# Kernel optimization log

Hardware: AMD Instinct MI355X
Metric: run time of the kernel (lower is better)

The kernel has to match this reference:

```python
import jax, jax.numpy as jnp
import numpy as np

K = 3  # kernel_size
PAD = K // 2


def setup_inputs() -> dict:
    key = jax.random.key(0)
    k1, k2 = jax.random.split(key)
    B, C, H, W = 8, 64, 128, 128
    x = jax.random.normal(k1, (B, C, H, W), dtype=jnp.float32)
    dynamic_kernel = jax.random.normal(k2, (B, C, K * K, H, W), dtype=jnp.float32)
    return {"x": x, "dynamic_kernel": dynamic_kernel}


def reference(x, dynamic_kernel):
    # x: [B,C,H,W]; dynamic_kernel: [B,C,K^2,H,W]
    B, C, H, W = x.shape
    xp = jnp.pad(x, ((0, 0), (0, 0), (PAD, PAD), (PAD, PAD)))
    # F.unfold patch ordering: (ki, kj) row-major, matching view(B,C,K*K,H,W)
    patches = jnp.stack(
        [xp[:, :, i:i + H, j:j + W] for i in range(K) for j in range(K)],
        axis=2,
    )  # [B,C,K^2,H,W]
    out = (patches * dynamic_kernel).sum(axis=2)  # [B,C,H,W]
    return out
```

## Files before the change

kernel.cpp:

```cpp
#include <hip/hip_runtime.h>


constexpr int Bc = 8, Cc = 64, Hc = 128, Wc = 128;
constexpr int HW = Hc * Wc;

__global__ __launch_bounds__(256) void adaconv2d_kernel(
    const float* __restrict__ x,
    const float* __restrict__ dk,
    float* __restrict__ out)
{
    int tid = blockIdx.x * blockDim.x + threadIdx.x;
    int w0   = (tid & 31) << 2;
    int rest = tid >> 5;
    int h    = rest & (Hc - 1);
    int bc   = rest >> 7;

    const float* xp = x + bc * HW;
    const float* kp = dk + (long long)bc * 9 * HW + h * Wc + w0;

    float xr[3][6];
    #pragma unroll
    for (int r = 0; r < 3; ++r) {
        int hh = h + r - 1;
        if (hh >= 0 && hh < Hc) {
            const float* row = xp + hh * Wc;
            float4 m = *reinterpret_cast<const float4*>(row + w0);
            xr[r][1] = m.x; xr[r][2] = m.y; xr[r][3] = m.z; xr[r][4] = m.w;
            xr[r][0] = (w0 > 0)        ? row[w0 - 1] : 0.f;
            xr[r][5] = (w0 + 4 < Wc)   ? row[w0 + 4] : 0.f;
        } else {
            #pragma unroll
            for (int j = 0; j < 6; ++j) xr[r][j] = 0.f;
        }
    }

    float4 acc = make_float4(0.f, 0.f, 0.f, 0.f);
    #pragma unroll
    for (int r = 0; r < 3; ++r) {
        #pragma unroll
        for (int s = 0; s < 3; ++s) {
            float4 k = *reinterpret_cast<const float4*>(kp + (r * 3 + s) * HW);
            acc.x += xr[r][s + 0] * k.x;
            acc.y += xr[r][s + 1] * k.y;
            acc.z += xr[r][s + 2] * k.z;
            acc.w += xr[r][s + 3] * k.w;
        }
    }

    *reinterpret_cast<float4*>(out + bc * HW + h * Wc + w0) = acc;
}

extern "C" void kernel_launch(void* const* d_in, const int* in_sizes, int n_in,
                              void* d_out, int out_size, void* d_ws, size_t ws_size,
                              hipStream_t stream) {
    const float* x  = (const float*)d_in[0];
    const float* dk = (const float*)d_in[1];
    float* out      = (float*)d_out;

    const int total_quads = Bc * Cc * Hc * (Wc / 4);
    const int block = 256;
    const int grid  = total_quads / block;
    adaconv2d_kernel<<<grid, block, 0, stream>>>(x, dk, out);
}
```

Before: 413.8 us.

## Process 16 outputs per thread with nontemporal kernel loads and output stores

Each thread now computes 8 contiguous columns for two rows 16 apart, and each block covers a 32-row chunk of one channel plane. The dynamic kernel weights are read and the outputs written with nontemporal builtins to avoid polluting cache with streamed data. The aim is more bytes in flight per thread and fewer redundant halo loads. The trade-off is four times fewer threads and higher register use, which may reduce occupancy.

```diff
diff --git a/kernel.cpp b/kernel.cpp
--- a/kernel.cpp
+++ b/kernel.cpp
@@ -3,51 +3,97 @@
 
 constexpr int Bc = 8, Cc = 64, Hc = 128, Wc = 128;
 constexpr int HW = Hc * Wc;
+constexpr int ROWS = 32;
+constexpr int CHUNKS = Hc / ROWS;
+
+typedef float f32x4 __attribute__((ext_vector_type(4)));
+
+__device__ __forceinline__ void load_xrows(const float* __restrict__ xp,
+                                           int R, int w0, float xr[3][10]) {
+    #pragma unroll
+    for (int r = 0; r < 3; ++r) {
+        int hh = R + r - 1;
+        if (hh >= 0 && hh < Hc) {
+            const float* row = xp + hh * Wc;
+            f32x4 m0 = *reinterpret_cast<const f32x4*>(row + w0);
+            f32x4 m1 = *reinterpret_cast<const f32x4*>(row + w0 + 4);
+            xr[r][1] = m0.x; xr[r][2] = m0.y; xr[r][3] = m0.z; xr[r][4] = m0.w;
+            xr[r][5] = m1.x; xr[r][6] = m1.y; xr[r][7] = m1.z; xr[r][8] = m1.w;
+            xr[r][0] = (w0 > 0)      ? row[w0 - 1] : 0.f;
+            xr[r][9] = (w0 + 8 < Wc) ? row[w0 + 8] : 0.f;
+        } else {
+            #pragma unroll
+            for (int q = 0; q < 10; ++q) xr[r][q] = 0.f;
+        }
+    }
+}
 
 __global__ __launch_bounds__(256) void adaconv2d_kernel(
     const float* __restrict__ x,
     const float* __restrict__ dk,
     float* __restrict__ out)
 {
-    int tid = blockIdx.x * blockDim.x + threadIdx.x;
-    int w0   = (tid & 31) << 2;
-    int rest = tid >> 5;
-    int h    = rest & (Hc - 1);
-    int bc   = rest >> 7;
+    int i  = threadIdx.x;
+    int j  = i & 15;
+    int p  = i >> 4;
+    int w0 = j << 3;
+
+    int blk = blockIdx.x;
+    int cb  = blk & (CHUNKS - 1);
+    int bc  = blk >> 2;
+
+    int R0 = cb * ROWS + p;
+    int R1 = R0 + 16;
 
     const float* xp = x + bc * HW;
-    const float* kp = dk + (long long)bc * 9 * HW + h * Wc + w0;
+    const float* kb = dk + (long long)bc * 9 * HW;
 
-    float xr[3][6];
+    float xa[3][10], xb[3][10];
+    load_xrows(xp, R0, w0, xa);
+    load_xrows(xp, R1, w0, xb);
+
+    float a0[8], a1[8];
     #pragma unroll
-    for (int r = 0; r < 3; ++r) {
-        int hh = h + r - 1;
-        if (hh >= 0 && hh < Hc) {
-            const float* row = xp + hh * Wc;
-            float4 m = *reinterpret_cast<const float4*>(row + w0);
-            xr[r][1] = m.x; xr[r][2] = m.y; xr[r][3] = m.z; xr[r][4] = m.w;
-            xr[r][0] = (w0 > 0)        ? row[w0 - 1] : 0.f;
-            xr[r][5] = (w0 + 4 < Wc)   ? row[w0 + 4] : 0.f;
-        } else {
-            #pragma unroll
-            for (int j = 0; j < 6; ++j) xr[r][j] = 0.f;
-        }
+    for (int q = 0; q < 8; ++q) { a0[q] = 0.f; a1[q] = 0.f; }
+
+    #pragma unroll
+    for (int t = 0; t < 9; ++t) {
+        const int r = t / 3, s = t - 3 * r;
+        const float* kt = kb + t * HW;
+        f32x4 k0a = __builtin_nontemporal_load(reinterpret_cast<const f32x4*>(kt + R0 * Wc + w0));
+        f32x4 k0b = __builtin_nontemporal_load(reinterpret_cast<const f32x4*>(kt + R0 * Wc + w0 + 4));
+        f32x4 k1a = __builtin_nontemporal_load(reinterpret_cast<const f32x4*>(kt + R1 * Wc + w0));
+        f32x4 k1b = __builtin_nontemporal_load(reinterpret_cast<const f32x4*>(kt + R1 * Wc + w0 + 4));
+
+        a0[0] += xa[r][s + 0] * k0a.x;
+        a0[1] += xa[r][s + 1] * k0a.y;
+        a0[2] += xa[r][s + 2] * k0a.z;
+        a0[3] += xa[r][s + 3] * k0a.w;
+        a0[4] += xa[r][s + 4] * k0b.x;
+        a0[5] += xa[r][s + 5] * k0b.y;
+        a0[6] += xa[r][s + 6] * k0b.z;
+        a0[7] += xa[r][s + 7] * k0b.w;
+
+        a1[0] += xb[r][s + 0] * k1a.x;
+        a1[1] += xb[r][s + 1] * k1a.y;
+        a1[2] += xb[r][s + 2] * k1a.z;
+        a1[3] += xb[r][s + 3] * k1a.w;
+        a1[4] += xb[r][s + 4] * k1b.x;
+        a1[5] += xb[r][s + 5] * k1b.y;
+        a1[6] += xb[r][s + 6] * k1b.z;
+        a1[7] += xb[r][s + 7] * k1b.w;
     }
 
-    float4 acc = make_float4(0.f, 0.f, 0.f, 0.f);
-    #pragma unroll
-    for (int r = 0; r < 3; ++r) {
-        #pragma unroll
-        for (int s = 0; s < 3; ++s) {
-            float4 k = *reinterpret_cast<const float4*>(kp + (r * 3 + s) * HW);
-            acc.x += xr[r][s + 0] * k.x;
-            acc.y += xr[r][s + 1] * k.y;
-            acc.z += xr[r][s + 2] * k.z;
-            acc.w += xr[r][s + 3] * k.w;
-        }
-    }
-
-    *reinterpret_cast<float4*>(out + bc * HW + h * Wc + w0) = acc;
+    float* o0 = out + bc * HW + R0 * Wc + w0;
+    float* o1 = out + bc * HW + R1 * Wc + w0;
+    f32x4 s0a = { a0[0], a0[1], a0[2], a0[3] };
+    f32x4 s0b = { a0[4], a0[5], a0[6], a0[7] };
+    f32x4 s1a = { a1[0], a1[1], a1[2], a1[3] };
+    f32x4 s1b = { a1[4], a1[5], a1[6], a1[7] };
+    __builtin_nontemporal_store(s0a, reinterpret_cast<f32x4*>(o0));
+    __builtin_nontemporal_store(s0b, reinterpret_cast<f32x4*>(o0 + 4));
+    __builtin_nontemporal_store(s1a, reinterpret_cast<f32x4*>(o1));
+    __builtin_nontemporal_store(s1b, reinterpret_cast<f32x4*>(o1 + 4));
 }
 
 extern "C" void kernel_launch(void* const* d_in, const int* in_sizes, int n_in,
@@ -57,8 +103,6 @@
     const float* dk = (const float*)d_in[1];
     float* out      = (float*)d_out;
 
-    const int total_quads = Bc * Cc * Hc * (Wc / 4);
-    const int block = 256;
-    const int grid  = total_quads / block;
-    adaconv2d_kernel<<<grid, block, 0, stream>>>(x, dk, out);
+    const int grid = Bc * Cc * CHUNKS;
+    adaconv2d_kernel<<<grid, 256, 0, stream>>>(x, dk, out);
 }
```

Result: slower. 433.8 us (+4.8%).
